# Kernel tuning notes

Measured on AMD Instinct MI355X. Metric: run time of the kernel, lower is better.

The kernel has to match this reference:

```python
import jax, jax.numpy as jnp
import numpy as np

N, E, DIN, HID, H, ED = 50000, 800000, 128, 64, 4, 5
Z_IDX = 3          # impedance column
PHYS_W = 1.0       # physics_weight
NEG_SLOPE = 0.2    # GATv2 leaky_relu slope


def gat_layer(x, src, dst, ea, Wl, bl, Wr, br, We, att, temp, bias, concat):
    """PhysicsGATv2Conv (add_self_loops=False, eval mode / no dropout)."""
    n = x.shape[0]
    Hh, C = att.shape
    xl = (x @ Wl + bl).reshape(n, Hh, C)   # lin_l -> source features
    xr = (x @ Wr + br).reshape(n, Hh, C)   # lin_r -> target features
    # physics-enhanced edge attr: overwrite last column with temp * w / |Z|
    z = jnp.clip(ea[:, Z_IDX], 1e-6, None)
    ea = ea.at[:, -1].set(temp * PHYS_W / z)
    e = (ea @ We).reshape(-1, Hh, C)       # lin_edge (no bias)
    m = jax.nn.leaky_relu(xl[src] + xr[dst] + e, NEG_SLOPE)  # [E,H,C]
    logit = jnp.einsum('ehc,hc->eh', m, att)                 # [E,H]
    # segment softmax over incoming edges of each target node
    lmax = jax.ops.segment_max(logit, dst, num_segments=n)
    w = jnp.exp(logit - lmax[dst])
    den = jax.ops.segment_sum(w, dst, num_segments=n)
    a = w / (den[dst] + 1e-16)
    out = jax.ops.segment_sum(xl[src] * a[:, :, None], dst, num_segments=n)
    out = out.reshape(n, Hh * C) if concat else out.mean(axis=1)
    return out + bias


def layer_norm(x, w, b):
    mu = x.mean(-1, keepdims=True)
    v = ((x - mu) ** 2).mean(-1, keepdims=True)
    return (x - mu) * jax.lax.rsqrt(v + 1e-5) * w + b


def setup_inputs() -> dict:
    key = jax.random.key(0)
    ks = iter(jax.random.split(key, 40))
    nk = lambda: next(ks)
    d = {}
    d['x'] = jax.random.normal(nk(), (N, DIN), jnp.float32)
    d['edge_index'] = jax.random.randint(nk(), (2, E), 0, N)
    d['edge_attr'] = jax.random.uniform(nk(), (E, ED), jnp.float32)
    hd = HID * H
    cfg = [(DIN, True), (hd, True), (hd, False)]
    for i, (din, concat) in enumerate(cfg):
        dout = hd if concat else HID
        d[f'Wl{i}'] = jax.random.normal(nk(), (din, hd), jnp.float32) / np.sqrt(din)
        d[f'bl{i}'] = 0.01 * jax.random.normal(nk(), (hd,), jnp.float32)
        d[f'Wr{i}'] = jax.random.normal(nk(), (din, hd), jnp.float32) / np.sqrt(din)
        d[f'br{i}'] = 0.01 * jax.random.normal(nk(), (hd,), jnp.float32)
        d[f'We{i}'] = jax.random.normal(nk(), (ED, hd), jnp.float32) / np.sqrt(ED)
        d[f'att{i}'] = jax.random.normal(nk(), (H, HID), jnp.float32) / np.sqrt(HID)
        d[f'temp{i}'] = jnp.float32(1.0)
        d[f'bias{i}'] = 0.01 * jax.random.normal(nk(), (dout,), jnp.float32)
        d[f'lnw{i}'] = jnp.ones((dout,), jnp.float32)
        d[f'lnb{i}'] = jnp.zeros((dout,), jnp.float32)
    d['pw0'] = jax.random.normal(nk(), (DIN, hd), jnp.float32) / np.sqrt(DIN)
    d['pb0'] = jnp.zeros((hd,), jnp.float32)
    d['pw2'] = jax.random.normal(nk(), (hd, HID), jnp.float32) / np.sqrt(hd)
    d['pb2'] = jnp.zeros((HID,), jnp.float32)
    return d


def reference(x, edge_index, edge_attr,
              Wl0, bl0, Wr0, br0, We0, att0, temp0, bias0, lnw0, lnb0,
              Wl1, bl1, Wr1, br1, We1, att1, temp1, bias1, lnw1, lnb1,
              Wl2, bl2, Wr2, br2, We2, att2, temp2, bias2, lnw2, lnb2,
              pw0, pb0, pw2, pb2):
    src, dst = edge_index[0], edge_index[1]
    # layer 0: 128 -> 256 (concat), residual projected
    h = gat_layer(x, src, dst, edge_attr, Wl0, bl0, Wr0, br0, We0, att0, temp0, bias0, True)
    h = layer_norm(h, lnw0, lnb0) + (x @ pw0 + pb0)
    h = jax.nn.elu(h)
    # layer 1: 256 -> 256 (concat), identity residual
    h1 = gat_layer(h, src, dst, edge_attr, Wl1, bl1, Wr1, br1, We1, att1, temp1, bias1, True)
    h = layer_norm(h1, lnw1, lnb1) + h
    h = jax.nn.elu(h)
    # layer 2: 256 -> 64 (head-mean), residual projected, no activation
    h2 = gat_layer(h, src, dst, edge_attr, Wl2, bl2, Wr2, br2, We2, att2, temp2, bias2, False)
    out = layer_norm(h2, lnw2, lnb2) + (h @ pw2 + pb2)
    return out
```

## Files before the change

kernel.cpp:

```cpp
#include <hip/hip_runtime.h>
#include <math.h>

#define NN 50000
#define EE 800000
#define NB 196

typedef _Float16 half8 __attribute__((ext_vector_type(8)));
typedef _Float16 hv4  __attribute__((ext_vector_type(4)));
typedef _Float16 hv2  __attribute__((ext_vector_type(2)));
typedef float floatx16 __attribute__((ext_vector_type(16)));
typedef float fv4 __attribute__((ext_vector_type(4)));

__device__ __forceinline__ float fexp2(float x) { return __builtin_amdgcn_exp2f(x); }

template<int CTRL>
__device__ __forceinline__ float dppadd(float x) {
    int t = __builtin_amdgcn_update_dpp(0, __float_as_int(x), CTRL, 0xf, 0xf, false);
    return x + __int_as_float(t);
}
__device__ __forceinline__ float red16(float x) {
    x = dppadd<0x121>(x);
    x = dppadd<0x122>(x);
    x = dppadd<0x124>(x);
    x = dppadd<0x128>(x);
    return x;
}

__global__ __launch_bounds__(256) void swizzleA(
    const float* __restrict__ A, _Float16* __restrict__ Asw, int M, int K)
{
    int wave = threadIdx.x >> 6, lane = threadIdx.x & 63;
    int tile = blockIdx.x;
    int kc = blockIdx.y * 4 + wave;
    int KC = K >> 4;
    if (kc >= KC) return;
    int row = tile * 32 + (lane & 31);
    int k0 = kc * 16 + (lane >> 5) * 8;
    float4 v0 = make_float4(0.f, 0.f, 0.f, 0.f);
    float4 v1 = make_float4(0.f, 0.f, 0.f, 0.f);
    if (row < M) {
        const float* p = A + (size_t)row * K + k0;
        v0 = *(const float4*)p;
        v1 = *(const float4*)(p + 4);
    }
    half8 o;
    o[0] = (_Float16)v0.x; o[1] = (_Float16)v0.y;
    o[2] = (_Float16)v0.z; o[3] = (_Float16)v0.w;
    o[4] = (_Float16)v1.x; o[5] = (_Float16)v1.y;
    o[6] = (_Float16)v1.z; o[7] = (_Float16)v1.w;
    *(half8*)(Asw + (((size_t)tile * KC + kc) * 64 + lane) * 8) = o;
}

__global__ __launch_bounds__(256) void prep_weights(
    const float* __restrict__ s0, const float* __restrict__ s1,
    const float* __restrict__ s2, const float* __restrict__ s3,
    const float* __restrict__ s4, const float* __restrict__ s5,
    const float* __restrict__ s6, const float* __restrict__ s7,
    _Float16* __restrict__ catB0, _Float16* __restrict__ catB1,
    _Float16* __restrict__ catB2,
    const float* __restrict__ bl0, const float* __restrict__ br0,
    const float* __restrict__ pb0, const float* __restrict__ bl1,
    const float* __restrict__ br1, const float* __restrict__ bl2,
    const float* __restrict__ br2, const float* __restrict__ pb2,
    float* __restrict__ cb0, float* __restrict__ cb1, float* __restrict__ cb2)
{
    int b = blockIdx.x;
    if (b >= 184) {
        int t = (b - 184) * 256 + threadIdx.x;
        if (t < 768) {
            cb0[t] = (t < 256) ? bl0[t] : (t < 512) ? br0[t - 256] : pb0[t - 512];
        } else if (t < 1280) {
            int u = t - 768;
            cb1[u] = (u < 256) ? bl1[u] : br1[u - 256];
        } else if (t < 1856) {
            int u = t - 1280;
            cb2[u] = (u < 256) ? bl2[u] : (u < 512) ? br2[u - 256] : pb2[u - 512];
        }
        return;
    }
    int wave = threadIdx.x >> 6, lane = threadIdx.x & 63;
    int pair = b * 4 + wave;
    const int cum[9] = {0, 64, 128, 192, 320, 448, 576, 704, 736};
    int job = 0;
    while (pair >= cum[job + 1]) ++job;
    const float* srcs[8] = {s0, s1, s2, s3, s4, s5, s6, s7};
    const int KCs[8] = {8, 8, 8, 16, 16, 16, 16, 16};
    const int NCs[8] = {256, 256, 256, 256, 256, 256, 256, 64};
    const int ntb[8] = {0, 8, 16, 0, 8, 0, 8, 16};
    _Float16* dsts[8] = {catB0, catB0, catB0, catB1, catB1, catB2, catB2, catB2};
    int p = pair - cum[job];
    int KC = KCs[job], NC = NCs[job];
    int nt = p / KC, kc = p - nt * KC;
    int n = (nt >> 1) * 64 + ((lane & 31) * 2) + (nt & 1);
    int k0 = kc * 16 + (lane >> 5) * 8;
    const float* B = srcs[job];
    half8 o;
#pragma unroll
    for (int jj = 0; jj < 8; ++jj)
        o[jj] = (_Float16)B[(size_t)(k0 + jj) * NC + n];
    int ntG = ntb[job] + nt;
    *(half8*)(dsts[job] + (((size_t)ntG * KC + kc) * 64 + lane) * 8) = o;
}

__global__ __launch_bounds__(256) void gemm_mfma(
    const _Float16* __restrict__ Asw, const _Float16* __restrict__ Bsw,
    const float* __restrict__ bias, _Float16* __restrict__ C,
    int M, int K, int NC)
{
    __shared__ _Float16 lb[16384];
    const int wave = threadIdx.x >> 6, lane = threadIdx.x & 63;
    const int KC = K >> 4;
    const int g = blockIdx.y;

    {
        const _Float16* srcB = Bsw + (size_t)(2 * g) * KC * 512;
        int total = 2 * KC * 512;
        for (int t = threadIdx.x * 8; t < total; t += 2048)
            *(half8*)(lb + t) = *(const half8*)(srcB + t);
    }
    __syncthreads();

    const int rt0 = blockIdx.x * 8 + wave * 2;
    const half8* Ap0 = (const half8*)Asw + (size_t)rt0 * KC * 64 + lane;
    const half8* Ap1 = Ap0 + (size_t)KC * 64;
    const half8* Bl0 = (const half8*)lb + lane;
    const half8* Bl1 = (const half8*)lb + (size_t)KC * 64 + lane;

    floatx16 accE0 = {0.f}, accE1 = {0.f}, accO0 = {0.f}, accO1 = {0.f};

#pragma unroll 4
    for (int kc = 0; kc < KC; ++kc) {
        half8 a0 = Ap0[(size_t)kc * 64];
        half8 a1 = Ap1[(size_t)kc * 64];
        half8 b0 = Bl0[(size_t)kc * 64];
        half8 b1 = Bl1[(size_t)kc * 64];
        accE0 = __builtin_amdgcn_mfma_f32_32x32x16_f16(a0, b0, accE0, 0, 0, 0);
        accE1 = __builtin_amdgcn_mfma_f32_32x32x16_f16(a1, b0, accE1, 0, 0, 0);
        accO0 = __builtin_amdgcn_mfma_f32_32x32x16_f16(a0, b1, accO0, 0, 0, 0);
        accO1 = __builtin_amdgcn_mfma_f32_32x32x16_f16(a1, b1, accO1, 0, 0, 0);
    }

    const int nlane = lane & 31, hs = lane >> 5;
    int colb = g * 64 + nlane * 2;
    float be = bias[colb], bo = bias[colb + 1];
#pragma unroll
    for (int r = 0; r < 16; ++r) {
        int rowin = (r & 3) + 8 * (r >> 2) + 4 * hs;
        int row0 = rt0 * 32 + rowin;
        int row1 = row0 + 32;
        if (row0 < M) {
            hv2 pe;
            pe[0] = (_Float16)(accE0[r] + be);
            pe[1] = (_Float16)(accO0[r] + bo);
            *(hv2*)(C + (size_t)row0 * NC + colb) = pe;
        }
        if (row1 < M) {
            hv2 po;
            po[0] = (_Float16)(accE1[r] + be);
            po[1] = (_Float16)(accO1[r] + bo);
            *(hv2*)(C + (size_t)row1 * NC + colb) = po;
        }
    }
}

__global__ __launch_bounds__(256) void hist_kernel(const int* __restrict__ dst,
                                                   int* __restrict__ deg)
{
    int e = blockIdx.x * 256 + threadIdx.x;
    if (e < EE) atomicAdd(&deg[dst[e]], 1);
}

__global__ __launch_bounds__(256) void scan_local(const int* __restrict__ deg,
                                                  int* __restrict__ rowoff,
                                                  int* __restrict__ part)
{
    __shared__ int sd[256];
    int tid = threadIdx.x;
    int i = blockIdx.x * 256 + tid;
    int v = (i < NN) ? deg[i] : 0;
    sd[tid] = v;
    __syncthreads();
    for (int off = 1; off < 256; off <<= 1) {
        int t = (tid >= off) ? sd[tid - off] : 0;
        __syncthreads();
        sd[tid] += t;
        __syncthreads();
    }
    if (i < NN) rowoff[i] = sd[tid] - v;
    if (tid == 255) part[blockIdx.x] = sd[255];
}

__global__ __launch_bounds__(256) void scan_part(int* __restrict__ part,
                                                 int* __restrict__ rowoff)
{
    __shared__ int sd[256];
    int tid = threadIdx.x;
    int v = (tid < NB) ? part[tid] : 0;
    sd[tid] = v;
    __syncthreads();
    for (int off = 1; off < 256; off <<= 1) {
        int t = (tid >= off) ? sd[tid - off] : 0;
        __syncthreads();
        sd[tid] += t;
        __syncthreads();
    }
    if (tid < NB) part[tid] = sd[tid] - v;
    if (tid == 0) rowoff[NN] = EE;
}

__global__ __launch_bounds__(256) void scan_add(int* __restrict__ rowoff,
                                                const int* __restrict__ part,
                                                int* __restrict__ cursor)
{
    int i = blockIdx.x * 256 + threadIdx.x;
    if (i < NN) {
        rowoff[i] += part[blockIdx.x];
        cursor[i] = 0;
    }
}

__global__ __launch_bounds__(256) void scatter_kernel(
    const int* __restrict__ src, const int* __restrict__ dst,
    const float* __restrict__ ea, const int* __restrict__ rowoff,
    int* __restrict__ cursor, int* __restrict__ srcp,
    float4* __restrict__ eap, float* __restrict__ erec)
{
    int e = blockIdx.x * 256 + threadIdx.x;
    if (e < EE) {
        int d = dst[e];
        int pos = rowoff[d] + atomicAdd(&cursor[d], 1);
        srcp[pos] = src[e];
        const float* p = ea + (size_t)e * 5;
        eap[pos] = make_float4(p[0], p[1], p[2], p[3]);
        erec[pos] = 1.0f / fmaxf(p[3], 1e-6f);
    }
}

template<int MODE, int RSTRIDE>
__global__ __launch_bounds__(256) void fused_attn_ln(
    const int* __restrict__ rowoff, const int* __restrict__ srcp,
    const float4* __restrict__ eap, const float* __restrict__ erec,
    const _Float16* __restrict__ xlp,
    const float* __restrict__ We, const float* __restrict__ att,
    const float* __restrict__ temp, const float* __restrict__ bias,
    const float* __restrict__ lnw, const float* __restrict__ lnb,
    const _Float16* __restrict__ residH, const float* __restrict__ residF,
    float* __restrict__ outF, _Float16* __restrict__ aswOut)
{
    int v = __builtin_amdgcn_readfirstlane(blockIdx.x * 4 + (threadIdx.x >> 6));
    int lane = threadIdx.x & 63;
    if (v >= NN) return;
    int grp = lane >> 4;
    int sub = lane & 15;
    int j = grp * 64 + sub * 4;

    fv4 ww0 = *(const fv4*)(We + j);
    fv4 ww1 = *(const fv4*)(We + 256 + j);
    fv4 ww2 = *(const fv4*)(We + 512 + j);
    fv4 ww3 = *(const fv4*)(We + 768 + j);
    fv4 ww4 = *(const fv4*)(We + 1024 + j);
    fv4 atv = *(const fv4*)(att + j);
    fv4 xrv = __builtin_convertvector(
        *(const hv4*)(xlp + (size_t)v * RSTRIDE + 256 + j), fv4);
    float tmp = temp[0];
    const float L2E = 1.44269504088896340736f;

    float mxd = -INFINITY, dend = 0.f;
    fv4 acc = {0.f, 0.f, 0.f, 0.f};

    int beg = rowoff[v], end = rowoff[v + 1];
    int i = beg;
    for (; i + 4 <= end; i += 4) {
        int s[4]; float4 a[4]; float q[4]; fv4 xv[4]; float l[4];
#pragma unroll
        for (int u = 0; u < 4; ++u) {
            s[u] = srcp[i + u];
            a[u] = eap[i + u];
            q[u] = tmp * erec[i + u];
        }
#pragma unroll
        for (int u = 0; u < 4; ++u)
            xv[u] = __builtin_convertvector(
                *(const hv4*)(xlp + (size_t)s[u] * RSTRIDE + j), fv4);
#pragma unroll
        for (int u = 0; u < 4; ++u) {
            fv4 m = xv[u] + xrv;
            m = m + a[u].x * ww0; m = m + a[u].y * ww1; m = m + a[u].z * ww2;
            m = m + a[u].w * ww3; m = m + q[u] * ww4;
            m = __builtin_elementwise_max(m, m * 0.2f);
            fv4 p = m * atv;
            l[u] = (p[0] + p[1]) + (p[2] + p[3]);
        }
#pragma unroll
        for (int u = 0; u < 4; ++u) l[u] = red16(l[u]) * L2E;
        float nm = fmaxf(fmaxf(l[0], l[1]), fmaxf(l[2], l[3]));
        nm = fmaxf(nm, mxd);
        float sc = fexp2(mxd - nm);
        float e0 = fexp2(l[0] - nm);
        float e1 = fexp2(l[1] - nm);
        float e2 = fexp2(l[2] - nm);
        float e3 = fexp2(l[3] - nm);
        mxd = nm;
        dend = dend * sc + ((e0 + e1) + (e2 + e3));
        acc = acc * sc +
              ((xv[0] * e0 + xv[1] * e1) + (xv[2] * e2 + xv[3] * e3));
    }
    for (; i < end; ++i) {
        int s0 = srcp[i];
        float4 a0 = eap[i];
        float q0 = tmp * erec[i];
        fv4 x0 = __builtin_convertvector(
            *(const hv4*)(xlp + (size_t)s0 * RSTRIDE + j), fv4);
        fv4 m0 = x0 + xrv;
        m0 = m0 + a0.x * ww0; m0 = m0 + a0.y * ww1; m0 = m0 + a0.z * ww2;
        m0 = m0 + a0.w * ww3; m0 = m0 + q0 * ww4;
        m0 = __builtin_elementwise_max(m0, m0 * 0.2f);
        fv4 p0 = m0 * atv;
        float l0 = (p0[0] + p0[1]) + (p0[2] + p0[3]);
        l0 = red16(l0) * L2E;
        float nm = fmaxf(mxd, l0);
        float sc = fexp2(mxd - nm);
        float e0 = fexp2(l0 - nm);
        mxd = nm;
        dend = dend * sc + e0;
        acc = acc * sc + x0 * e0;
    }

    float inv = __builtin_amdgcn_rcpf(dend + 1e-16f);
    if (MODE <= 1) {
        fv4 bb = *(const fv4*)(bias + j);
        fv4 o = acc * inv + bb;
        float s  = (o[0] + o[1]) + (o[2] + o[3]);
        fv4 oq = o * o;
        float s2 = (oq[0] + oq[1]) + (oq[2] + oq[3]);
        s = red16(s);   s += __shfl_xor(s, 16, 64);  s += __shfl_xor(s, 32, 64);
        s2 = red16(s2); s2 += __shfl_xor(s2, 16, 64); s2 += __shfl_xor(s2, 32, 64);
        float mu = s * (1.f / 256.f);
        float var = s2 * (1.f / 256.f) - mu * mu;
        float rs = __builtin_amdgcn_rsqf(var + 1e-5f);
        fv4 lw = *(const fv4*)(lnw + j);
        fv4 lb = *(const fv4*)(lnb + j);
        fv4 rr;
        if (MODE == 0)
            rr = __builtin_convertvector(
                *(const hv4*)(residH + (size_t)v * RSTRIDE + j), fv4);
        else
            rr = *(const fv4*)(residF + (size_t)v * 256 + j);
        fv4 y = (o - mu) * rs * lw + lb + rr;
        y[0] = (y[0] > 0.f) ? y[0] : fexp2(y[0] * L2E) - 1.f;
        y[1] = (y[1] > 0.f) ? y[1] : fexp2(y[1] * L2E) - 1.f;
        y[2] = (y[2] > 0.f) ? y[2] : fexp2(y[2] * L2E) - 1.f;
        y[3] = (y[3] > 0.f) ? y[3] : fexp2(y[3] * L2E) - 1.f;
        if (MODE == 0)
            *(fv4*)(outF + (size_t)v * 256 + j) = y;
        int kc = j >> 4, half = (j >> 3) & 1, off = j & 7;
        size_t idx = (((size_t)(v >> 5) * 16 + kc) * 64 + (v & 31) + 32 * half) * 8 + off;
        hv4 yh = __builtin_convertvector(y, hv4);
        *(hv4*)(aswOut + idx) = yh;
    } else {
        fv4 r = acc * inv;
        r[0] += __shfl_xor(r[0], 16, 64); r[0] += __shfl_xor(r[0], 32, 64);
        r[1] += __shfl_xor(r[1], 16, 64); r[1] += __shfl_xor(r[1], 32, 64);
        r[2] += __shfl_xor(r[2], 16, 64); r[2] += __shfl_xor(r[2], 32, 64);
        r[3] += __shfl_xor(r[3], 16, 64); r[3] += __shfl_xor(r[3], 32, 64);
        fv4 bb = *(const fv4*)(bias + sub * 4);
        fv4 o = r * 0.25f + bb;
        float s  = (o[0] + o[1]) + (o[2] + o[3]);
        fv4 oq = o * o;
        float s2 = (oq[0] + oq[1]) + (oq[2] + oq[3]);
        s = red16(s);
        s2 = red16(s2);
        float mu = s * (1.f / 64.f);
        float var = s2 * (1.f / 64.f) - mu * mu;
        float rs = __builtin_amdgcn_rsqf(var + 1e-5f);
        fv4 lw = *(const fv4*)(lnw + sub * 4);
        fv4 lb = *(const fv4*)(lnb + sub * 4);
        fv4 rr = __builtin_convertvector(
            *(const hv4*)(residH + (size_t)v * RSTRIDE + sub * 4), fv4);
        fv4 y = (o - mu) * rs * lw + lb + rr;
        if (grp == 0)
            *(fv4*)(outF + (size_t)v * 64 + sub * 4) = y;
    }
}

extern "C" void kernel_launch(void* const* d_in, const int* in_sizes, int n_in,
                              void* d_out, int out_size, void* d_ws, size_t ws_size,
                              hipStream_t stream)
{
    const float* x    = (const float*)d_in[0];
    const int*   eidx = (const int*)d_in[1];
    const float* ea   = (const float*)d_in[2];
    const int* src = eidx;
    const int* dst = eidx + EE;

    const float *Wl[3], *bl[3], *Wr[3], *br[3], *We[3], *att[3], *temp[3],
                *bias[3], *lnw[3], *lnb[3];
    for (int i = 0; i < 3; ++i) {
        int b = 3 + i * 10;
        Wl[i]   = (const float*)d_in[b + 0];
        bl[i]   = (const float*)d_in[b + 1];
        Wr[i]   = (const float*)d_in[b + 2];
        br[i]   = (const float*)d_in[b + 3];
        We[i]   = (const float*)d_in[b + 4];
        att[i]  = (const float*)d_in[b + 5];
        temp[i] = (const float*)d_in[b + 6];
        bias[i] = (const float*)d_in[b + 7];
        lnw[i]  = (const float*)d_in[b + 8];
        lnb[i]  = (const float*)d_in[b + 9];
    }
    const float* pw0 = (const float*)d_in[33];
    const float* pb0 = (const float*)d_in[34];
    const float* pw2 = (const float*)d_in[35];
    const float* pb2 = (const float*)d_in[36];

    char* w = (char*)d_ws;
    float* h     = (float*)w; w += (size_t)NN * 256 * 4;
    char*  gbase = w;         w += (size_t)NN * 256 * 4;
    _Float16* xlr = (_Float16*)w; w += (size_t)NN * 768 * 2;
    float4* eap  = (float4*)w; w += (size_t)EE * 16;
    float* erec  = (float*)w; w += (size_t)EE * 4;
    int* srcp    = (int*)w;   w += (size_t)EE * 4;
    int* rowoff  = (int*)w;   w += (size_t)(NN + 16) * 4;
    int* cursor  = (int*)w;   w += (size_t)NN * 4;
    int* part    = (int*)w;   w += 1024;
    w = (char*)(((uintptr_t)w + 255) & ~(uintptr_t)255);
    _Float16* catB0 = (_Float16*)w; w += 196608;
    _Float16* catB1 = (_Float16*)w; w += 262144;
    _Float16* catB2 = (_Float16*)w; w += 294912;
    float* cb0 = (float*)w; w += 768 * 4;
    float* cb1 = (float*)w; w += 512 * 4;
    float* cb2 = (float*)w; w += 576 * 4;
    _Float16* Asw = (_Float16*)gbase;

    dim3 blk(256);
    dim3 grid_e((EE + 255) / 256);
    dim3 grid_nw((NN + 3) / 4);
    dim3 grid_nb(NB);
    const int RB = 196;

    hipMemsetAsync(cursor, 0, (size_t)NN * 4, stream);
    hipLaunchKernelGGL(hist_kernel, grid_e, blk, 0, stream, dst, cursor);
    hipLaunchKernelGGL(scan_local, grid_nb, blk, 0, stream, cursor, rowoff, part);
    hipLaunchKernelGGL(scan_part, dim3(1), blk, 0, stream, part, rowoff);
    hipLaunchKernelGGL(scan_add, grid_nb, blk, 0, stream, rowoff, part, cursor);
    hipLaunchKernelGGL(scatter_kernel, grid_e, blk, 0, stream,
                       src, dst, ea, rowoff, cursor, srcp, eap, erec);

    hipLaunchKernelGGL(prep_weights, dim3(192), blk, 0, stream,
                       Wl[0], Wr[0], pw0, Wl[1], Wr[1], Wl[2], Wr[2], pw2,
                       catB0, catB1, catB2,
                       bl[0], br[0], pb0, bl[1], br[1], bl[2], br[2], pb2,
                       cb0, cb1, cb2);

    swizzleA<<<dim3(1568, 2), blk, 0, stream>>>(x, Asw, NN, 128);
    gemm_mfma<<<dim3(RB, 12), blk, 0, stream>>>(
        Asw, catB0, cb0, xlr, NN, 128, 768);
    fused_attn_ln<0, 768><<<grid_nw, blk, 0, stream>>>(
        rowoff, srcp, eap, erec, xlr, We[0], att[0], temp[0],
        bias[0], lnw[0], lnb[0], xlr + 512, nullptr, h, Asw);

    gemm_mfma<<<dim3(RB, 8), blk, 0, stream>>>(
        Asw, catB1, cb1, xlr, NN, 256, 512);
    fused_attn_ln<1, 512><<<grid_nw, blk, 0, stream>>>(
        rowoff, srcp, eap, erec, xlr, We[1], att[1], temp[1],
        bias[1], lnw[1], lnb[1], nullptr, h, nullptr, Asw);

    gemm_mfma<<<dim3(RB, 9), blk, 0, stream>>>(
        Asw, catB2, cb2, xlr, NN, 256, 576);
    fused_attn_ln<2, 576><<<grid_nw, blk, 0, stream>>>(
        rowoff, srcp, eap, erec, xlr, We[2], att[2], temp[2],
        bias[2], lnw[2], lnb[2], xlr + 512, nullptr, (float*)d_out, nullptr);
}
```

Baseline: 676.9 us.

## Drop LDS staging in MFMA GEMM and scalarize edge indices in attention

The GEMM no longer copies B tiles into shared memory behind a barrier. Each wave now reads B directly from global memory for its own column group, with a 2x2 wave layout per block covering fewer row tiles and two column groups, and the grid is reshaped to match. In the attention kernel, the row offsets and source indices are wrapped in readfirstlane so that gather addresses are computed as scalars. The trade is less LDS use and no barrier in exchange for more global and L2 traffic on B. Clamping g for odd column-group counts makes duplicate waves write identical outputs redundantly.

```diff
diff --git a/kernel.cpp b/kernel.cpp
--- a/kernel.cpp
+++ b/kernel.cpp
@@ -107,24 +107,17 @@
     const float* __restrict__ bias, _Float16* __restrict__ C,
     int M, int K, int NC)
 {
-    __shared__ _Float16 lb[16384];
     const int wave = threadIdx.x >> 6, lane = threadIdx.x & 63;
     const int KC = K >> 4;
-    const int g = blockIdx.y;
-
-    {
-        const _Float16* srcB = Bsw + (size_t)(2 * g) * KC * 512;
-        int total = 2 * KC * 512;
-        for (int t = threadIdx.x * 8; t < total; t += 2048)
-            *(half8*)(lb + t) = *(const half8*)(srcB + t);
-    }
-    __syncthreads();
-
-    const int rt0 = blockIdx.x * 8 + wave * 2;
+    const int rt0 = blockIdx.x * 4 + (wave & 1) * 2;
+    const int NG = NC >> 6;
+    int g = blockIdx.y * 2 + (wave >> 1);
+    if (g >= NG) g = NG - 1;
+
     const half8* Ap0 = (const half8*)Asw + (size_t)rt0 * KC * 64 + lane;
     const half8* Ap1 = Ap0 + (size_t)KC * 64;
-    const half8* Bl0 = (const half8*)lb + lane;
-    const half8* Bl1 = (const half8*)lb + (size_t)KC * 64 + lane;
+    const half8* Bp0 = (const half8*)Bsw + (size_t)(2 * g) * KC * 64 + lane;
+    const half8* Bp1 = Bp0 + (size_t)KC * 64;
 
     floatx16 accE0 = {0.f}, accE1 = {0.f}, accO0 = {0.f}, accO1 = {0.f};
 
@@ -132,8 +125,8 @@
     for (int kc = 0; kc < KC; ++kc) {
         half8 a0 = Ap0[(size_t)kc * 64];
         half8 a1 = Ap1[(size_t)kc * 64];
-        half8 b0 = Bl0[(size_t)kc * 64];
-        half8 b1 = Bl1[(size_t)kc * 64];
+        half8 b0 = Bp0[(size_t)kc * 64];
+        half8 b1 = Bp1[(size_t)kc * 64];
         accE0 = __builtin_amdgcn_mfma_f32_32x32x16_f16(a0, b0, accE0, 0, 0, 0);
         accE1 = __builtin_amdgcn_mfma_f32_32x32x16_f16(a1, b0, accE1, 0, 0, 0);
         accO0 = __builtin_amdgcn_mfma_f32_32x32x16_f16(a0, b1, accO0, 0, 0, 0);
@@ -268,13 +261,14 @@
     float mxd = -INFINITY, dend = 0.f;
     fv4 acc = {0.f, 0.f, 0.f, 0.f};
 
-    int beg = rowoff[v], end = rowoff[v + 1];
+    int beg = __builtin_amdgcn_readfirstlane(rowoff[v]);
+    int end = __builtin_amdgcn_readfirstlane(rowoff[v + 1]);
     int i = beg;
     for (; i + 4 <= end; i += 4) {
         int s[4]; float4 a[4]; float q[4]; fv4 xv[4]; float l[4];
 #pragma unroll
         for (int u = 0; u < 4; ++u) {
-            s[u] = srcp[i + u];
+            s[u] = __builtin_amdgcn_readfirstlane(srcp[i + u]);
             a[u] = eap[i + u];
             q[u] = tmp * erec[i + u];
         }
@@ -306,7 +300,7 @@
               ((xv[0] * e0 + xv[1] * e1) + (xv[2] * e2 + xv[3] * e3));
     }
     for (; i < end; ++i) {
-        int s0 = srcp[i];
+        int s0 = __builtin_amdgcn_readfirstlane(srcp[i]);
         float4 a0 = eap[i];
         float q0 = tmp * erec[i];
         fv4 x0 = __builtin_convertvector(
@@ -436,7 +430,7 @@
     dim3 grid_e((EE + 255) / 256);
     dim3 grid_nw((NN + 3) / 4);
     dim3 grid_nb(NB);
-    const int RB = 196;
+    const int MT = 391;
 
     hipMemsetAsync(cursor, 0, (size_t)NN * 4, stream);
     hipLaunchKernelGGL(hist_kernel, grid_e, blk, 0, stream, dst, cursor);
@@ -452,20 +446,20 @@
                        bl[0], br[0], pb0, bl[1], br[1], bl[2], br[2], pb2,
                        cb0, cb1, cb2);
 
-    swizzleA<<<dim3(1568, 2), blk, 0, stream>>>(x, Asw, NN, 128);
-    gemm_mfma<<<dim3(RB, 12), blk, 0, stream>>>(
+    swizzleA<<<dim3(1564, 2), blk, 0, stream>>>(x, Asw, NN, 128);
+    gemm_mfma<<<dim3(MT, 6), blk, 0, stream>>>(
         Asw, catB0, cb0, xlr, NN, 128, 768);
     fused_attn_ln<0, 768><<<grid_nw, blk, 0, stream>>>(
         rowoff, srcp, eap, erec, xlr, We[0], att[0], temp[0],
         bias[0], lnw[0], lnb[0], xlr + 512, nullptr, h, Asw);
 
-    gemm_mfma<<<dim3(RB, 8), blk, 0, stream>>>(
+    gemm_mfma<<<dim3(MT, 4), blk, 0, stream>>>(
         Asw, catB1, cb1, xlr, NN, 256, 512);
     fused_attn_ln<1, 512><<<grid_nw, blk, 0, stream>>>(
         rowoff, srcp, eap, erec, xlr, We[1], att[1], temp[1],
         bias[1], lnw[1], lnb[1], nullptr, h, nullptr, Asw);
 
-    gemm_mfma<<<dim3(RB, 9), blk, 0, stream>>>(
+    gemm_mfma<<<dim3(MT, 5), blk, 0, stream>>>(
         Asw, catB2, cb2, xlr, NN, 256, 576);
     fused_attn_ln<2, 576><<<grid_nw, blk, 0, stream>>>(
         rowoff, srcp, eap, erec, xlr, We[2], att[2], temp[2],
```

Measured after the change: 635.4 us. 6.1% less time.
